# Kernel optimization log

Measured on AMD Instinct MI355X. Metric: run time of the kernel, lower is better.

The kernel has to match this reference:

```python
import jax, jax.numpy as jnp
import numpy as np

B, T, H, E = 256, 512, 512, 32

def setup_inputs() -> dict:
    key = jax.random.key(0)
    ks = jax.random.split(key, 7)
    events = jax.random.randint(ks[0], (B, T), 0, E, dtype=jnp.int32)
    # strictly increasing event times (as produced by cumsum of positive gaps upstream)
    gaps = jax.random.uniform(ks[1], (B, T), dtype=jnp.float32) * 0.1 + 1e-3
    times = jnp.cumsum(gaps, axis=1)
    emb = jax.random.normal(ks[2], (E, H), dtype=jnp.float32) * 0.05
    # 5 gate Linears (input, forget, output, cell, decay) stacked: [2H, 5H]
    W_gates = jax.random.normal(ks[3], (2 * H, 5 * H), dtype=jnp.float32) * (1.0 / np.sqrt(2 * H))
    b_gates = jnp.zeros((5 * H,), dtype=jnp.float32)
    W_int = jax.random.normal(ks[4], (H, E), dtype=jnp.float32) * (1.0 / np.sqrt(H))
    b_int = jnp.zeros((E,), dtype=jnp.float32)
    return {"events": events, "times": times, "emb": emb,
            "W_gates": W_gates, "b_gates": b_gates, "W_int": W_int, "b_int": b_int}

def reference(events, times, emb, W_gates, b_gates, W_int, b_int):
    Bs, Ts = events.shape
    Hs = emb.shape[1]
    x_seq = emb[events]                                   # [B,T,H] embedding lookup
    deltas = jnp.concatenate([times[:, :1], jnp.diff(times, axis=1)], axis=1)  # [B,T]
    xs = (jnp.transpose(x_seq, (1, 0, 2)), deltas.T)      # ([T,B,H], [T,B])

    def step(carry, inp):
        h, c = carry
        x, dt = inp
        comb = jnp.concatenate([x, h], axis=1)            # [B,2H]
        g = comb @ W_gates + b_gates                      # [B,5H] fused gate GEMM
        i, f, o, c_tilde, d = jnp.split(g, 5, axis=1)
        i, f, o, c_tilde = jnp.tanh(i), jnp.tanh(f), jnp.tanh(o), jnp.tanh(c_tilde)
        decay = jax.nn.softplus(d)
        c_dec = c * jnp.exp(-decay * dt[:, None])
        c_n = f * c_dec + i * c_tilde
        h_n = o * jnp.tanh(c_n)
        lam = jax.nn.softplus(h_n @ W_int + b_int)        # [B,E]
        return (h_n, c_n), (lam, h_n)

    h0 = jnp.zeros((Bs, Hs), dtype=times.dtype)
    c0 = jnp.zeros((Bs, Hs), dtype=times.dtype)
    _, (lams, hs) = jax.lax.scan(step, (h0, c0), xs)
    intensities = jnp.transpose(lams, (1, 0, 2))          # [B,T,E]
    hidden_states = jnp.transpose(hs, (1, 0, 2))          # [B,T,H]
    return intensities, hidden_states
```

## Files before the change

kernel.cpp:

```cpp
#include <hip/hip_runtime.h>
#include <math.h>


#define Bb   256
#define Tt   512
#define Hh   512
#define Ee   32
#define G5H  2560
#define NTHR 256
#define RT   16
#define CT   32

typedef __attribute__((ext_vector_type(8))) short f16x8;
typedef __attribute__((ext_vector_type(4))) float f32x4;
typedef __attribute__((ext_vector_type(4))) unsigned u32x4;
typedef __attribute__((ext_vector_type(2))) unsigned u32x2;

__device__ __forceinline__ float softplusf(float x) {
    return fmaxf(x, 0.f) + __logf(1.f + __expf(-fabsf(x)));
}
__device__ __forceinline__ float fast_tanh(float x) {
    const float t = fminf(fmaxf(x, -15.f), 15.f);
    const float e = __expf(2.f * t);
    return (e - 1.f) / (e + 1.f);
}
__device__ __forceinline__ unsigned short f2h(float f) {
    _Float16 h = (_Float16)f;
    return *reinterpret_cast<unsigned short*>(&h);
}

__device__ __forceinline__ void load_slow8(const unsigned* p, u32x4 (&d)[8]) {
    asm volatile(
        "global_load_dwordx4 %0, %8, off sc0 sc1\n\t"
        "global_load_dwordx4 %1, %8, off offset:16 sc0 sc1\n\t"
        "global_load_dwordx4 %2, %8, off offset:128 sc0 sc1\n\t"
        "global_load_dwordx4 %3, %8, off offset:144 sc0 sc1\n\t"
        "global_load_dwordx4 %4, %8, off offset:256 sc0 sc1\n\t"
        "global_load_dwordx4 %5, %8, off offset:272 sc0 sc1\n\t"
        "global_load_dwordx4 %6, %8, off offset:384 sc0 sc1\n\t"
        "global_load_dwordx4 %7, %8, off offset:400 sc0 sc1\n\t"
        "s_waitcnt vmcnt(0)"
        : "=&v"(d[0]), "=&v"(d[1]), "=&v"(d[2]), "=&v"(d[3]),
          "=&v"(d[4]), "=&v"(d[5]), "=&v"(d[6]), "=&v"(d[7])
        : "v"(p) : "memory");
}
__device__ __forceinline__ void st_tag(unsigned* p, unsigned data, unsigned tag) {
    u32x2 v; v.x = data; v.y = tag;
    asm volatile("global_store_dwordx2 %0, %1, off sc0 sc1"
                 :: "v"(p), "v"(v) : "memory");
}

__global__ __launch_bounds__(NTHR, 1)
void nhp_scan(const int* __restrict__ events, const float* __restrict__ times,
              const float* __restrict__ emb, const float* __restrict__ Wg,
              const float* __restrict__ bg, float* __restrict__ out_hid,
              unsigned* __restrict__ hbs) {
    __shared__ float red[4][10][16][18];
    __shared__ float gx[Ee][5][34];
    __shared__ float dt_lds[RT][516];
    __shared__ unsigned char ev_lds[RT][520];

    const int tid  = threadIdx.x, bid = blockIdx.x;
    const int rt   = bid & 15;
    const int ct   = bid >> 4;
    const int r0   = rt * RT;
    const int lane = tid & 63;
    const int ks   = tid >> 6;
    const int frow = lane & 15, kgrp = lane >> 4;
    const int erow = tid >> 4;
    const int ecp  = (tid & 15) * 2;

    for (int u = tid; u < RT * Tt; u += NTHR) {
        const int row = u >> 9, pp = u & 511;
        const float t1 = times[(r0 + row) * Tt + pp];
        const float t0 = pp ? times[(r0 + row) * Tt + pp - 1] : 0.f;
        dt_lds[row][pp] = t1 - t0;
        ev_lds[row][pp] = (unsigned char)events[(r0 + row) * Tt + pp];
    }

    for (int u = tid; u < Ee * 5 * CT; u += NTHR) {
        const int e = u / 160, r = u - e * 160;
        const int g = r >> 5, hc = r & 31;
        const int gcol = g * Hh + ct * CT + hc;
        float acc = bg[gcol];
        const float* er = emb + (size_t)e * Hh;
        for (int k = 0; k < Hh; k += 4) {
            acc += er[k]     * Wg[(size_t)k       * G5H + gcol];
            acc += er[k + 1] * Wg[(size_t)(k + 1) * G5H + gcol];
            acc += er[k + 2] * Wg[(size_t)(k + 2) * G5H + gcol];
            acc += er[k + 3] * Wg[(size_t)(k + 3) * G5H + gcol];
        }
        gx[e][g][hc ^ ((e & 7) << 2)] = acc;
    }

    f16x8 Bf[10][4];
    #pragma unroll
    for (int n = 0; n < 10; ++n) {
        const int col = (n >> 1) * Hh + ct * CT + (n & 1) * 16 + frow;
        #pragma unroll
        for (int kk = 0; kk < 4; ++kk) {
            const int k0 = ks * 128 + kk * 32 + kgrp * 8;
            union { f16x8 v; unsigned u[4]; } tmp;
            #pragma unroll
            for (int r = 0; r < 4; ++r) {
                const float w0 = Wg[(size_t)(Hh + k0 + 2 * r)     * G5H + col];
                const float w1 = Wg[(size_t)(Hh + k0 + 2 * r + 1) * G5H + col];
                tmp.u[r] = (unsigned)f2h(w0) | ((unsigned)f2h(w1) << 16);
            }
            Bf[n][kk] = tmp.v;
        }
    }

    float cA = 0.f, cB = 0.f;
    float2 prev_hn;
    __syncthreads();

    for (int p = 0; p < Tt; ++p) {
        if (p > 0) {
            const size_t off = ((size_t)((p - 1) & 1) * Bb * 256
                             + (size_t)(r0 + frow) * 256 + ks * 64 + kgrp * 4) * 2;
            const unsigned want = (unsigned)p;
            u32x4 d[8];
            int guard = 0;
            for (;;) {
                load_slow8(hbs + off, d);
                int ok = 1;
                #pragma unroll
                for (int i = 0; i < 8; ++i)
                    ok &= (d[i].y == want) & (d[i].w == want);
                if (__all(ok)) break;
                if (++guard > 100000) break;
                __builtin_amdgcn_s_sleep(1);
            }

            *(float2*)(out_hid + ((size_t)(r0 + erow) * Tt + (p - 1)) * Hh
                       + ct * CT + ecp) = prev_hn;

            f16x8 a[4];
            #pragma unroll
            for (int kk = 0; kk < 4; ++kk) {
                union { f16x8 v; unsigned u[4]; } t;
                t.u[0] = d[2 * kk].x;     t.u[1] = d[2 * kk].z;
                t.u[2] = d[2 * kk + 1].x; t.u[3] = d[2 * kk + 1].z;
                a[kk] = t.v;
            }
            f32x4 acc[10];
            #pragma unroll
            for (int n = 0; n < 10; ++n) acc[n] = (f32x4){0.f, 0.f, 0.f, 0.f};
            #pragma unroll
            for (int kk = 0; kk < 4; ++kk) {
                #pragma unroll
                for (int n = 0; n < 10; ++n)
                    acc[n] = __builtin_amdgcn_mfma_f32_16x16x32_f16(
                        a[kk], Bf[n][kk], acc[n], 0, 0, 0);
            }
            __syncthreads();
            #pragma unroll
            for (int n = 0; n < 10; ++n)
                #pragma unroll
                for (int r = 0; r < 4; ++r)
                    red[ks][n][kgrp * 4 + r][frow] = acc[n][r];
            __syncthreads();
        }

        const int   e  = ev_lds[erow][p];
        const float dt = dt_lds[erow][p];
        const int   sc = (e & 7) << 2;
        float hn[2];
        {
            float v0[5], v1[5];
            const int tl0 = ecp >> 4, fc = ecp & 15;
            #pragma unroll
            for (int gt = 0; gt < 5; ++gt) {
                const float2 gv = *(const float2*)&gx[e][gt][ecp ^ sc];
                v0[gt] = gv.x; v1[gt] = gv.y;
                if (p > 0) {
                    const int tl = gt * 2 + tl0;
                    #pragma unroll
                    for (int s = 0; s < 4; ++s) {
                        const float2 pr = *(const float2*)&red[s][tl][erow][fc];
                        v0[gt] += pr.x; v1[gt] += pr.y;
                    }
                }
            }
            #pragma unroll
            for (int q = 0; q < 2; ++q) {
                const float* v = q ? v1 : v0;
                const float ig  = fast_tanh(v[0]);
                const float fg  = fast_tanh(v[1]);
                const float og  = fast_tanh(v[2]);
                const float ctl = fast_tanh(v[3]);
                const float dec = softplusf(v[4]);
                const float cpv = q ? cB : cA;
                const float cn  = fg * (cpv * __expf(-dec * dt)) + ig * ctl;
                if (q) cB = cn; else cA = cn;
                hn[q] = og * fast_tanh(cn);
            }
        }

        const unsigned pk = (unsigned)f2h(hn[0]) | ((unsigned)f2h(hn[1]) << 16);
        st_tag(hbs + ((size_t)(p & 1) * Bb * 256 + (size_t)(r0 + erow) * 256
                      + ct * 16 + (ecp >> 1)) * 2, pk, (unsigned)(p + 1));

        prev_hn.x = hn[0]; prev_hn.y = hn[1];
    }
    *(float2*)(out_hid + ((size_t)(r0 + erow) * Tt + (Tt - 1)) * Hh
               + ct * CT + ecp) = prev_hn;
}

__global__ __launch_bounds__(NTHR)
void nhp_intens(const float* __restrict__ out_hid, const float* __restrict__ Wi,
                const float* __restrict__ bi, float* __restrict__ out_int) {
    const int tid  = threadIdx.x;
    const int w    = tid >> 6;
    const int lane = tid & 63;
    const int col  = lane & 15, kgrp = lane >> 4;

    f16x8 Bfi[2][16];
    #pragma unroll
    for (int n = 0; n < 2; ++n)
        #pragma unroll
        for (int kk = 0; kk < 16; ++kk) {
            const int k0 = kk * 32 + kgrp * 8;
            union { f16x8 v; unsigned u[4]; } tmp;
            #pragma unroll
            for (int r = 0; r < 4; ++r) {
                const float w0 = Wi[(size_t)(k0 + 2 * r)     * Ee + n * 16 + col];
                const float w1 = Wi[(size_t)(k0 + 2 * r + 1) * Ee + n * 16 + col];
                tmp.u[r] = (unsigned)f2h(w0) | ((unsigned)f2h(w1) << 16);
            }
            Bfi[n][kk] = tmp.v;
        }
    const float bv[2] = { bi[col], bi[16 + col] };

    #pragma unroll
    for (int it = 0; it < 2; ++it) {
        const size_t rowbase = (size_t)blockIdx.x * 128 + (w * 2 + it) * 16;
        f32x4 acc0 = (f32x4){0.f,0.f,0.f,0.f}, acc1 = acc0;
        #pragma unroll
        for (int kk = 0; kk < 16; ++kk) {
            const float* hp = out_hid + (rowbase + (lane & 15)) * Hh + kk * 32 + kgrp * 8;
            const float4 hA = *(const float4*)hp;
            const float4 hB = *(const float4*)(hp + 4);
            union { f16x8 v; unsigned u[4]; } t;
            t.u[0] = (unsigned)f2h(hA.x) | ((unsigned)f2h(hA.y) << 16);
            t.u[1] = (unsigned)f2h(hA.z) | ((unsigned)f2h(hA.w) << 16);
            t.u[2] = (unsigned)f2h(hB.x) | ((unsigned)f2h(hB.y) << 16);
            t.u[3] = (unsigned)f2h(hB.z) | ((unsigned)f2h(hB.w) << 16);
            acc0 = __builtin_amdgcn_mfma_f32_16x16x32_f16(t.v, Bfi[0][kk], acc0, 0, 0, 0);
            acc1 = __builtin_amdgcn_mfma_f32_16x16x32_f16(t.v, Bfi[1][kk], acc1, 0, 0, 0);
        }
        #pragma unroll
        for (int i = 0; i < 4; ++i) {
            const size_t row = rowbase + kgrp * 4 + i;
            out_int[row * Ee + col]      = softplusf(acc0[i] + bv[0]);
            out_int[row * Ee + 16 + col] = softplusf(acc1[i] + bv[1]);
        }
    }
}

extern "C" void kernel_launch(void* const* d_in, const int* in_sizes, int n_in,
                              void* d_out, int out_size, void* d_ws, size_t ws_size,
                              hipStream_t stream) {
    const int*   events = (const int*)d_in[0];
    const float* times  = (const float*)d_in[1];
    const float* emb    = (const float*)d_in[2];
    const float* Wg     = (const float*)d_in[3];
    const float* bg     = (const float*)d_in[4];
    const float* Wi     = (const float*)d_in[5];
    const float* bi     = (const float*)d_in[6];
    float* out_int = (float*)d_out;
    float* out_hid = out_int + (size_t)Bb * Tt * Ee;
    unsigned* hbs = (unsigned*)((char*)d_ws + 4096);

    hipMemsetAsync(hbs, 0, (size_t)2 * Bb * 256 * 8, stream);
    hipLaunchKernelGGL(nhp_scan, dim3(256), dim3(NTHR), 0, stream,
                       events, times, emb, Wg, bg, out_hid, hbs);
    hipLaunchKernelGGL(nhp_intens, dim3((Bb * Tt) / 128), dim3(NTHR), 0, stream,
                       out_hid, Wi, bi, out_int);
}
```

Baseline: 2.505 ms.

## Replace per-element tagged h exchange with per-block flags and packed h buffer

Cross-block hidden-state exchange no longer carries a step tag next to every fp16 pair. Each block now writes packed fp16 h into a plain buffer, drains its stores, and thread 0 publishes a per-block step flag. Consumers poll a few flags and then issue four dense 16-byte loads, where before they polled eight tagged loads of mostly tag data. This halves exchange traffic and shortens polling, at the cost of an extra block barrier, a store drain and a flag store on every step, which adds latency to the serial chain.

```diff
diff --git a/kernel.cpp b/kernel.cpp
--- a/kernel.cpp
+++ b/kernel.cpp
@@ -13,8 +13,6 @@
 
 typedef __attribute__((ext_vector_type(8))) short f16x8;
 typedef __attribute__((ext_vector_type(4))) float f32x4;
-typedef __attribute__((ext_vector_type(4))) unsigned u32x4;
-typedef __attribute__((ext_vector_type(2))) unsigned u32x2;
 
 __device__ __forceinline__ float softplusf(float x) {
     return fmaxf(x, 0.f) + __logf(1.f + __expf(-fabsf(x)));
@@ -29,32 +27,32 @@
     return *reinterpret_cast<unsigned short*>(&h);
 }
 
-__device__ __forceinline__ void load_slow8(const unsigned* p, u32x4 (&d)[8]) {
+__device__ __forceinline__ void load_a4(const unsigned short* p, f16x8 (&a)[4]) {
     asm volatile(
-        "global_load_dwordx4 %0, %8, off sc0 sc1\n\t"
-        "global_load_dwordx4 %1, %8, off offset:16 sc0 sc1\n\t"
-        "global_load_dwordx4 %2, %8, off offset:128 sc0 sc1\n\t"
-        "global_load_dwordx4 %3, %8, off offset:144 sc0 sc1\n\t"
-        "global_load_dwordx4 %4, %8, off offset:256 sc0 sc1\n\t"
-        "global_load_dwordx4 %5, %8, off offset:272 sc0 sc1\n\t"
-        "global_load_dwordx4 %6, %8, off offset:384 sc0 sc1\n\t"
-        "global_load_dwordx4 %7, %8, off offset:400 sc0 sc1\n\t"
+        "global_load_dwordx4 %0, %4, off sc0 sc1\n\t"
+        "global_load_dwordx4 %1, %4, off offset:64 sc0 sc1\n\t"
+        "global_load_dwordx4 %2, %4, off offset:128 sc0 sc1\n\t"
+        "global_load_dwordx4 %3, %4, off offset:192 sc0 sc1\n\t"
         "s_waitcnt vmcnt(0)"
-        : "=&v"(d[0]), "=&v"(d[1]), "=&v"(d[2]), "=&v"(d[3]),
-          "=&v"(d[4]), "=&v"(d[5]), "=&v"(d[6]), "=&v"(d[7])
+        : "=&v"(a[0]), "=&v"(a[1]), "=&v"(a[2]), "=&v"(a[3])
         : "v"(p) : "memory");
 }
-__device__ __forceinline__ void st_tag(unsigned* p, unsigned data, unsigned tag) {
-    u32x2 v; v.x = data; v.y = tag;
-    asm volatile("global_store_dwordx2 %0, %1, off sc0 sc1"
+__device__ __forceinline__ void st_u32_sc(void* p, unsigned v) {
+    asm volatile("global_store_dword %0, %1, off sc0 sc1"
                  :: "v"(p), "v"(v) : "memory");
+}
+__device__ __forceinline__ unsigned ld_u32_sc(const unsigned* p) {
+    unsigned v;
+    asm volatile("global_load_dword %0, %1, off sc0 sc1\n\ts_waitcnt vmcnt(0)"
+                 : "=v"(v) : "v"(p) : "memory");
+    return v;
 }
 
 __global__ __launch_bounds__(NTHR, 1)
 void nhp_scan(const int* __restrict__ events, const float* __restrict__ times,
               const float* __restrict__ emb, const float* __restrict__ Wg,
               const float* __restrict__ bg, float* __restrict__ out_hid,
-              unsigned* __restrict__ hbs) {
+              unsigned* __restrict__ flags, unsigned short* __restrict__ hb) {
     __shared__ float red[4][10][16][18];
     __shared__ float gx[Ee][5][34];
     __shared__ float dt_lds[RT][516];
@@ -112,38 +110,25 @@
     }
 
     float cA = 0.f, cB = 0.f;
-    float2 prev_hn;
     __syncthreads();
 
     for (int p = 0; p < Tt; ++p) {
         if (p > 0) {
-            const size_t off = ((size_t)((p - 1) & 1) * Bb * 256
-                             + (size_t)(r0 + frow) * 256 + ks * 64 + kgrp * 4) * 2;
+            const unsigned* fp = flags + rt * 16 + ks * 4 + (lane & 3);
             const unsigned want = (unsigned)p;
-            u32x4 d[8];
             int guard = 0;
             for (;;) {
-                load_slow8(hbs + off, d);
-                int ok = 1;
-                #pragma unroll
-                for (int i = 0; i < 8; ++i)
-                    ok &= (d[i].y == want) & (d[i].w == want);
-                if (__all(ok)) break;
-                if (++guard > 100000) break;
+                const unsigned fv = ld_u32_sc(fp);
+                if (__all(fv >= want)) break;
+                if (++guard > 300000) break;
                 __builtin_amdgcn_s_sleep(1);
             }
 
-            *(float2*)(out_hid + ((size_t)(r0 + erow) * Tt + (p - 1)) * Hh
-                       + ct * CT + ecp) = prev_hn;
-
+            const unsigned short* hp = hb + (size_t)((p - 1) & 1) * Bb * Hh
+                                     + (size_t)(r0 + frow) * Hh + ks * 128 + kgrp * 8;
             f16x8 a[4];
-            #pragma unroll
-            for (int kk = 0; kk < 4; ++kk) {
-                union { f16x8 v; unsigned u[4]; } t;
-                t.u[0] = d[2 * kk].x;     t.u[1] = d[2 * kk].z;
-                t.u[2] = d[2 * kk + 1].x; t.u[3] = d[2 * kk + 1].z;
-                a[kk] = t.v;
-            }
+            load_a4(hp, a);
+
             f32x4 acc[10];
             #pragma unroll
             for (int n = 0; n < 10; ++n) acc[n] = (f32x4){0.f, 0.f, 0.f, 0.f};
@@ -154,14 +139,13 @@
                     acc[n] = __builtin_amdgcn_mfma_f32_16x16x32_f16(
                         a[kk], Bf[n][kk], acc[n], 0, 0, 0);
             }
-            __syncthreads();
             #pragma unroll
             for (int n = 0; n < 10; ++n)
                 #pragma unroll
                 for (int r = 0; r < 4; ++r)
                     red[ks][n][kgrp * 4 + r][frow] = acc[n][r];
-            __syncthreads();
-        }
+        }
+        __syncthreads();
 
         const int   e  = ev_lds[erow][p];
         const float dt = dt_lds[erow][p];
@@ -198,14 +182,16 @@
             }
         }
 
+        float2 ho; ho.x = hn[0]; ho.y = hn[1];
+        *(float2*)(out_hid + ((size_t)(r0 + erow) * Tt + p) * Hh + ct * CT + ecp) = ho;
         const unsigned pk = (unsigned)f2h(hn[0]) | ((unsigned)f2h(hn[1]) << 16);
-        st_tag(hbs + ((size_t)(p & 1) * Bb * 256 + (size_t)(r0 + erow) * 256
-                      + ct * 16 + (ecp >> 1)) * 2, pk, (unsigned)(p + 1));
-
-        prev_hn.x = hn[0]; prev_hn.y = hn[1];
-    }
-    *(float2*)(out_hid + ((size_t)(r0 + erow) * Tt + (Tt - 1)) * Hh
-               + ct * CT + ecp) = prev_hn;
+        st_u32_sc(hb + (size_t)(p & 1) * Bb * Hh
+                     + (size_t)(r0 + erow) * Hh + ct * CT + ecp, pk);
+
+        asm volatile("s_waitcnt vmcnt(0)" ::: "memory");
+        __syncthreads();
+        if (tid == 0) st_u32_sc(&flags[rt * 16 + ct], (unsigned)(p + 1));
+    }
 }
 
 __global__ __launch_bounds__(NTHR)
@@ -271,11 +257,12 @@
     const float* bi     = (const float*)d_in[6];
     float* out_int = (float*)d_out;
     float* out_hid = out_int + (size_t)Bb * Tt * Ee;
-    unsigned* hbs = (unsigned*)((char*)d_ws + 4096);
-
-    hipMemsetAsync(hbs, 0, (size_t)2 * Bb * 256 * 8, stream);
+    unsigned* flags = (unsigned*)d_ws;
+    unsigned short* hb = (unsigned short*)((char*)d_ws + 4096);
+
+    hipMemsetAsync(flags, 0, 4096, stream);
     hipLaunchKernelGGL(nhp_scan, dim3(256), dim3(NTHR), 0, stream,
-                       events, times, emb, Wg, bg, out_hid, hbs);
+                       events, times, emb, Wg, bg, out_hid, flags, hb);
     hipLaunchKernelGGL(nhp_intens, dim3((Bb * Tt) / 128), dim3(NTHR), 0, stream,
                        out_hid, Wi, bi, out_int);
 }
```

After: 2.266 ms, median of 2. 1.11x faster.

## Add per-wave flag polling with speculative tagged load and double-buffered reduction LDS

Applied to the files above, without the earlier changes.

Cross-block hand-off of the hidden state is restructured. Each wave first tries one speculative read of the tagged h buffer. If that read is stale, it polls compact per-wave progress flags and only then reloads the data, instead of spinning on the full 8x16-byte tagged load. The reduction LDS buffer is double-buffered by step parity, which drops one __syncthreads per step. The hidden-state output store now happens in the same step rather than being deferred. The cost is an extra flag store per wave per step, preceded by a full vmcnt wait, which may lengthen the critical path.

```diff
diff --git a/kernel.cpp b/kernel.cpp
--- a/kernel.cpp
+++ b/kernel.cpp
@@ -29,7 +29,7 @@
     return *reinterpret_cast<unsigned short*>(&h);
 }
 
-__device__ __forceinline__ void load_slow8(const unsigned* p, u32x4 (&d)[8]) {
+__device__ __forceinline__ void load_tagged8(const unsigned* p, u32x4 (&d)[8]) {
     asm volatile(
         "global_load_dwordx4 %0, %8, off sc0 sc1\n\t"
         "global_load_dwordx4 %1, %8, off offset:16 sc0 sc1\n\t"
@@ -49,13 +49,23 @@
     asm volatile("global_store_dwordx2 %0, %1, off sc0 sc1"
                  :: "v"(p), "v"(v) : "memory");
 }
+__device__ __forceinline__ void st_u32_sc(void* p, unsigned v) {
+    asm volatile("global_store_dword %0, %1, off sc0 sc1"
+                 :: "v"(p), "v"(v) : "memory");
+}
+__device__ __forceinline__ unsigned ld_u32_sc(const unsigned* p) {
+    unsigned v;
+    asm volatile("global_load_dword %0, %1, off sc0 sc1\n\ts_waitcnt vmcnt(0)"
+                 : "=v"(v) : "v"(p) : "memory");
+    return v;
+}
 
 __global__ __launch_bounds__(NTHR, 1)
 void nhp_scan(const int* __restrict__ events, const float* __restrict__ times,
               const float* __restrict__ emb, const float* __restrict__ Wg,
               const float* __restrict__ bg, float* __restrict__ out_hid,
-              unsigned* __restrict__ hbs) {
-    __shared__ float red[4][10][16][18];
+              unsigned* __restrict__ flags, unsigned* __restrict__ hb) {
+    __shared__ float red[2][4][10][16][18];
     __shared__ float gx[Ee][5][34];
     __shared__ float dt_lds[RT][516];
     __shared__ unsigned char ev_lds[RT][520];
@@ -112,29 +122,47 @@
     }
 
     float cA = 0.f, cB = 0.f;
-    float2 prev_hn;
+    int spec = 1;
     __syncthreads();
 
     for (int p = 0; p < Tt; ++p) {
+        const int par = p & 1;
         if (p > 0) {
-            const size_t off = ((size_t)((p - 1) & 1) * Bb * 256
-                             + (size_t)(r0 + frow) * 256 + ks * 64 + kgrp * 4) * 2;
+            const size_t off = ((size_t)(((p - 1) & 1) * Bb + (r0 + frow)) * 256
+                               + ks * 64 + kgrp * 4) * 2;
             const unsigned want = (unsigned)p;
             u32x4 d[8];
-            int guard = 0;
-            for (;;) {
-                load_slow8(hbs + off, d);
+            int need = 1;
+            if (spec) {
+                load_tagged8(hb + off, d);
                 int ok = 1;
                 #pragma unroll
                 for (int i = 0; i < 8; ++i)
                     ok &= (d[i].y == want) & (d[i].w == want);
-                if (__all(ok)) break;
-                if (++guard > 100000) break;
-                __builtin_amdgcn_s_sleep(1);
-            }
-
-            *(float2*)(out_hid + ((size_t)(r0 + erow) * Tt + (p - 1)) * Hh
-                       + ct * CT + ecp) = prev_hn;
+                if (__all(ok)) need = 0;
+            }
+            if (need) {
+                const unsigned* fp = flags + rt * 64 + ks * 16 + (lane & 15);
+                int guard = 0;
+                for (;;) {
+                    const unsigned fv = ld_u32_sc(fp);
+                    if (__all(fv >= want)) break;
+                    if (++guard > 300000) break;
+                    __builtin_amdgcn_s_sleep(1);
+                }
+                guard = 0;
+                for (;;) {
+                    load_tagged8(hb + off, d);
+                    int ok = 1;
+                    #pragma unroll
+                    for (int i = 0; i < 8; ++i)
+                        ok &= (d[i].y == want) & (d[i].w == want);
+                    if (__all(ok)) break;
+                    if (++guard > 100000) break;
+                    __builtin_amdgcn_s_sleep(1);
+                }
+            }
+            spec = need ? (spec ? 0 : 1) : 1;
 
             f16x8 a[4];
             #pragma unroll
@@ -154,14 +182,13 @@
                     acc[n] = __builtin_amdgcn_mfma_f32_16x16x32_f16(
                         a[kk], Bf[n][kk], acc[n], 0, 0, 0);
             }
-            __syncthreads();
             #pragma unroll
             for (int n = 0; n < 10; ++n)
                 #pragma unroll
                 for (int r = 0; r < 4; ++r)
-                    red[ks][n][kgrp * 4 + r][frow] = acc[n][r];
-            __syncthreads();
-        }
+                    red[par][ks][n][kgrp * 4 + r][frow] = acc[n][r];
+        }
+        __syncthreads();
 
         const int   e  = ev_lds[erow][p];
         const float dt = dt_lds[erow][p];
@@ -178,7 +205,7 @@
                     const int tl = gt * 2 + tl0;
                     #pragma unroll
                     for (int s = 0; s < 4; ++s) {
-                        const float2 pr = *(const float2*)&red[s][tl][erow][fc];
+                        const float2 pr = *(const float2*)&red[par][s][tl][erow][fc];
                         v0[gt] += pr.x; v1[gt] += pr.y;
                     }
                 }
@@ -198,14 +225,16 @@
             }
         }
 
+        float2 ho; ho.x = hn[0]; ho.y = hn[1];
+        *(float2*)(out_hid + ((size_t)(r0 + erow) * Tt + p) * Hh + ct * CT + ecp) = ho;
         const unsigned pk = (unsigned)f2h(hn[0]) | ((unsigned)f2h(hn[1]) << 16);
-        st_tag(hbs + ((size_t)(p & 1) * Bb * 256 + (size_t)(r0 + erow) * 256
-                      + ct * 16 + (ecp >> 1)) * 2, pk, (unsigned)(p + 1));
-
-        prev_hn.x = hn[0]; prev_hn.y = hn[1];
-    }
-    *(float2*)(out_hid + ((size_t)(r0 + erow) * Tt + (Tt - 1)) * Hh
-               + ct * CT + ecp) = prev_hn;
+        st_tag(hb + ((size_t)(par * Bb + (r0 + erow)) * 256
+                     + ct * 16 + (ecp >> 1)) * 2, pk, (unsigned)(p + 1));
+
+        asm volatile("s_waitcnt vmcnt(0)" ::: "memory");
+        if (lane == 0)
+            st_u32_sc(&flags[rt * 64 + ct * 4 + ks], (unsigned)(p + 1));
+    }
 }
 
 __global__ __launch_bounds__(NTHR)
@@ -271,11 +300,12 @@
     const float* bi     = (const float*)d_in[6];
     float* out_int = (float*)d_out;
     float* out_hid = out_int + (size_t)Bb * Tt * Ee;
-    unsigned* hbs = (unsigned*)((char*)d_ws + 4096);
-
-    hipMemsetAsync(hbs, 0, (size_t)2 * Bb * 256 * 8, stream);
+    unsigned* flags = (unsigned*)d_ws;
+    unsigned* hb = (unsigned*)((char*)d_ws + 4096);
+
+    hipMemsetAsync(d_ws, 0, 4096 + (size_t)2 * Bb * 256 * 8, stream);
     hipLaunchKernelGGL(nhp_scan, dim3(256), dim3(NTHR), 0, stream,
-                       events, times, emb, Wg, bg, out_hid, hbs);
+                       events, times, emb, Wg, bg, out_hid, flags, hb);
     hipLaunchKernelGGL(nhp_intens, dim3((Bb * Tt) / 128), dim3(NTHR), 0, stream,
                        out_hid, Wi, bi, out_int);
 }
```

New measurement: 3.270 ms. +30.5%, slower.
